# Performance work log

Hardware: AMD Instinct MI355X
Metric: run time of the kernel (lower is better)

Reference implementation:

```python
import jax, jax.numpy as jnp
import numpy as np

B, T, C, H = 2, 2048, 2048, 16
D = C // H  # head size = 128
ROPE_BASE = 10000.0


def setup_inputs() -> dict:
    key = jax.random.key(0)
    k1, k2, k3 = jax.random.split(key, 3)
    scale = 1.0 / np.sqrt(C)
    x = jax.random.normal(k1, (B, T, C), dtype=jnp.float32)
    w_qkv = jax.random.normal(k2, (3 * C, C), dtype=jnp.float32) * scale
    w_o = jax.random.normal(k3, (C, C), dtype=jnp.float32) * scale
    # rope cache: complex exp(i * pos * theta_j), stored as cos/sin, shape [T, D//2]
    inv_freq = 1.0 / (ROPE_BASE ** (np.arange(0, D, 2, dtype=np.float32) / D))  # [D//2]
    angles = np.arange(T, dtype=np.float32)[:, None] * inv_freq[None, :]        # [T, D//2]
    rope_cos = jnp.asarray(np.cos(angles))
    rope_sin = jnp.asarray(np.sin(angles))
    return {"x": x, "w_qkv": w_qkv, "w_o": w_o, "rope_cos": rope_cos, "rope_sin": rope_sin}


def _apply_rope(x, cos, sin):
    # x: [B, T, H, D]; cos/sin: [T, D//2]
    xr = x.reshape(*x.shape[:-1], D // 2, 2)
    x0, x1 = xr[..., 0], xr[..., 1]
    c = cos[None, :, None, :]
    s = sin[None, :, None, :]
    # complex multiply (x0 + i x1) * (c + i s)
    out = jnp.stack([x0 * c - x1 * s, x0 * s + x1 * c], axis=-1)
    return out.reshape(x.shape)


def reference(x, w_qkv, w_o, rope_cos, rope_sin):
    Bs, Ts, Cs = x.shape
    qkv = jnp.einsum('btc,ec->bte', x, w_qkv)  # [B, T, 3C]
    q, k, v = jnp.split(qkv, 3, axis=-1)
    q = q.reshape(Bs, Ts, H, D)
    k = k.reshape(Bs, Ts, H, D)
    v = v.reshape(Bs, Ts, H, D)
    q = _apply_rope(q, rope_cos[:Ts], rope_sin[:Ts])
    k = _apply_rope(k, rope_cos[:Ts], rope_sin[:Ts])
    scores = jnp.einsum('bthd,bshd->bhts', q, k) / jnp.sqrt(jnp.float32(D))
    causal = jnp.tril(jnp.ones((Ts, Ts), dtype=bool))
    scores = jnp.where(causal[None, None], scores, jnp.finfo(scores.dtype).min)
    attn = jax.nn.softmax(scores, axis=-1)
    y = jnp.einsum('bhts,bshd->bthd', attn, v).reshape(Bs, Ts, Cs)
    return jnp.einsum('btc,oc->bto', y, w_o)
```

## Files before the change

kernel.cpp:

```cpp
#include <hip/hip_runtime.h>
#include <cstdint>
#include <cstddef>

#define DEVI __device__ __forceinline__

typedef __attribute__((ext_vector_type(8))) short short8;
typedef __attribute__((ext_vector_type(4))) float f32x4;
typedef __attribute__((ext_vector_type(16))) float f32x16;
typedef __attribute__((ext_vector_type(4))) unsigned int u32x4;

static constexpr int Bdim = 2, T = 2048, C = 2048, H = 16, D = 128;
static constexpr int CQ = 3 * C;

DEVI unsigned short f2bf(float f) {
  unsigned int u = __float_as_uint(f);
  u = (u + 0x7fffu + ((u >> 16) & 1u)) >> 16;
  return (unsigned short)u;
}
DEVI float bf2f(unsigned int u) { return __uint_as_float(u << 16); }

DEVI unsigned int cvtpk(float lo, float hi) {
  unsigned int r;
  asm("v_cvt_pk_bf16_f32 %0, %1, %2" : "=v"(r) : "v"(lo), "v"(hi));
  return r;
}

DEVI void gload_lds16(const void* g, void* l) {
  __builtin_amdgcn_global_load_lds((const __attribute__((address_space(1))) void*)g,
                                   (__attribute__((address_space(3))) void*)l, 16, 0, 0);
}

__global__ __launch_bounds__(256) void convert_all(const float* __restrict__ x,
                                                   const float* __restrict__ wqkv,
                                                   const float* __restrict__ wo,
                                                   unsigned short* __restrict__ xb,
                                                   unsigned short* __restrict__ wqkvb,
                                                   unsigned short* __restrict__ wob) {
  int bid = blockIdx.x;
  const float* src;
  unsigned short* dst;
  if (bid < 8192) {
    src = x; dst = xb;
  } else if (bid < 8192 + 12288) {
    bid -= 8192; src = wqkv; dst = wqkvb;
  } else {
    bid -= 8192 + 12288; src = wo; dst = wob;
  }
  const int i = (bid * 256 + threadIdx.x) * 4;
  float4 v = *(const float4*)&src[i];
  uint2 o;
  o.x = (unsigned)f2bf(v.x) | ((unsigned)f2bf(v.y) << 16);
  o.y = (unsigned)f2bf(v.z) | ((unsigned)f2bf(v.w) << 16);
  *(uint2*)&dst[i] = o;
}

template <int OUT_BF16>
__global__ __launch_bounds__(256) void gemm_bt(const unsigned short* __restrict__ A,
                                               const unsigned short* __restrict__ Bm,
                                               void* __restrict__ outp,
                                               int M, int N, int Kd) {
  __shared__ __align__(16) unsigned short lds_a[128 * 64];
  __shared__ __align__(16) unsigned short lds_b[128 * 64];
  const int tid = threadIdx.x;
  const int wid = tid >> 6, lane = tid & 63;
  const int lg = lane >> 4, lc = lane & 15;
  const int m0 = blockIdx.y * 128, n0 = blockIdx.x * 128;
  const int wr = (wid >> 1) * 64, wc = (wid & 1) * 64;
  const int srow = wid * 8 + (lane >> 3);
  const int schunk = lane & 7;

  f32x4 acc[4][4] = {};

  for (int k0 = 0; k0 < Kd; k0 += 64) {
    __syncthreads();
#pragma unroll
    for (int j = 0; j < 4; ++j) {
      const int row = j * 32 + srow;
      const int cc = schunk ^ (row & 7);
      gload_lds16(&A[(size_t)(m0 + row) * Kd + k0 + cc * 8], &lds_a[j * 2048 + wid * 512]);
      gload_lds16(&Bm[(size_t)(n0 + row) * Kd + k0 + cc * 8], &lds_b[j * 2048 + wid * 512]);
    }
    __syncthreads();
    __builtin_amdgcn_s_setprio(1);
#pragma unroll
    for (int kk = 0; kk < 2; ++kk) {
      short8 af[4], bf[4];
#pragma unroll
      for (int m = 0; m < 4; ++m) {
        const int row = wr + m * 16 + lc;
        af[m] = *(const short8*)&lds_a[row * 64 + (((kk * 4 + lg) ^ (row & 7)) * 8)];
      }
#pragma unroll
      for (int n = 0; n < 4; ++n) {
        const int row = wc + n * 16 + lc;
        bf[n] = *(const short8*)&lds_b[row * 64 + (((kk * 4 + lg) ^ (row & 7)) * 8)];
      }
#pragma unroll
      for (int m = 0; m < 4; ++m)
#pragma unroll
        for (int n = 0; n < 4; ++n)
          acc[m][n] = __builtin_amdgcn_mfma_f32_16x16x32_bf16(af[m], bf[n], acc[m][n], 0, 0, 0);
    }
    __builtin_amdgcn_s_setprio(0);
  }

#pragma unroll
  for (int m = 0; m < 4; ++m)
#pragma unroll
    for (int n = 0; n < 4; ++n)
#pragma unroll
      for (int r = 0; r < 4; ++r) {
        const int row = m0 + wr + m * 16 + lg * 4 + r;
        const int col = n0 + wc + n * 16 + lc;
        const float v = acc[m][n][r];
        if (OUT_BF16)
          ((unsigned short*)outp)[(size_t)row * N + col] = f2bf(v);
        else
          ((float*)outp)[(size_t)row * N + col] = v;
      }
}

__global__ __launch_bounds__(256) void rope_vt_kernel(const unsigned short* __restrict__ qkv,
                                                      const float* __restrict__ cosb,
                                                      const float* __restrict__ sinb,
                                                      unsigned short* __restrict__ Qr,
                                                      unsigned short* __restrict__ Kr,
                                                      unsigned short* __restrict__ Vt) {
  if (blockIdx.x < 16384) {
    const int idx = blockIdx.x * 256 + threadIdx.x;
    const int i = idx & 63;
    const int h = (idx >> 6) & (H - 1);
    const int tg = idx >> 10;
    const int t = tg & (T - 1);
    const int b = tg >> 11;
    const float c = cosb[t * 64 + i], s = sinb[t * 64 + i];
    const unsigned short* row = qkv + (size_t)tg * CQ;
    const unsigned int q = *(const unsigned int*)&row[h * D + 2 * i];
    const unsigned int k = *(const unsigned int*)&row[C + h * D + 2 * i];
    const float q0 = bf2f(q & 0xffffu), q1 = bf2f(q >> 16);
    const float k0 = bf2f(k & 0xffffu), k1 = bf2f(k >> 16);
    const float SC = 0.08838834764831845f * 1.4426950408889634f;
    const float q0r = (q0 * c - q1 * s) * SC, q1r = (q0 * s + q1 * c) * SC;
    const float k0r = k0 * c - k1 * s, k1r = k0 * s + k1 * c;
    const size_t off = ((size_t)(b * H + h) * T + t) * D + 2 * i;
    *(unsigned int*)&Qr[off] = (unsigned)f2bf(q0r) | ((unsigned)f2bf(q1r) << 16);
    *(unsigned int*)&Kr[off] = (unsigned)f2bf(k0r) | ((unsigned)f2bf(k1r) << 16);
  } else {
    __shared__ unsigned short tile[64][65];
    const int bid2 = blockIdx.x - 16384;
    const int t0 = (bid2 & 31) * 64;
    const int d0 = ((bid2 >> 5) & 1) * 64;
    const int bh = bid2 >> 6, b = bh >> 4, h = bh & (H - 1);
    const int tx = threadIdx.x & 63, ty = threadIdx.x >> 6;
#pragma unroll
    for (int rr = 0; rr < 64; rr += 4)
      tile[rr + ty][tx] = qkv[(size_t)(b * T + t0 + rr + ty) * CQ + 2 * C + h * D + d0 + tx];
    __syncthreads();
#pragma unroll
    for (int rr = 0; rr < 64; rr += 4)
      Vt[((size_t)bh * D + d0 + rr + ty) * T + t0 + tx] = tile[tx][rr + ty];
  }
}

__global__ __launch_bounds__(256, 2) void flash_attn(const unsigned short* __restrict__ Q,
                                                     const unsigned short* __restrict__ K,
                                                     const unsigned short* __restrict__ Vt,
                                                     unsigned short* __restrict__ OA,
                                                     unsigned short* __restrict__ OB,
                                                     float2* __restrict__ ml) {
  __shared__ __align__(16) unsigned short ldsK[64 * 128];
  __shared__ __align__(16) unsigned short ldsV[64 * 128];

  const int bid = blockIdx.x;
  const int lid = (bid & 7) * 128 + (bid >> 3);
  const int bh = lid >> 5;
  const int qt = 15 - ((lid >> 1) & 15);
  const int hf = lid & 1;
  const int wid = threadIdx.x >> 6;
  const int lane = threadIdx.x & 63;
  const int l31 = lane & 31, l15 = lane & 15;
  const int hi = lane >> 5;
  const int b = bh >> 4, h = bh & (H - 1);
  const int q0w = qt * 128 + wid * 32;
  const int qrow = q0w + l31;

  const unsigned short* Qh = Q + (size_t)bh * T * D;
  const unsigned short* Kh = K + (size_t)bh * T * D;
  const unsigned short* Vh = Vt + (size_t)bh * D * T;

  const int sr = lane >> 4;
  const int tstart = hf ? (qt + 1) : 0;
  const int tend = hf ? (2 * qt + 2) : (qt + 1);

  short8 qf[8];
#pragma unroll
  for (int ds = 0; ds < 8; ++ds)
    qf[ds] = *(const short8*)&Qh[(size_t)qrow * D + ds * 16 + hi * 8];

  f32x16 oacc[4] = {};
  float m_run = -1e30f, l_run = 0.f;

  u32x4 rK[4], rV[4];

#pragma unroll
  for (int j = 0; j < 4; ++j) {
    const int r0 = (wid * 4 + j) * 4;
    const int row = r0 + sr;
    const int cc = l15 ^ (row & 15);
    rK[j] = *(const u32x4*)&Kh[(size_t)(tstart * 64 + row) * D + cc * 8];
    const int d = row + ((cc >> 3) << 6);
    rV[j] = *(const u32x4*)&Vh[(size_t)d * T + tstart * 64 + (cc & 7) * 8];
  }

  for (int t = tstart; t < tend; ++t) {
    const int kv0 = t * 64;

    __builtin_amdgcn_s_barrier();

#pragma unroll
    for (int j = 0; j < 4; ++j) {
      const int r0 = (wid * 4 + j) * 4;
      *(u32x4*)((char*)ldsK + r0 * 256 + lane * 16) = rK[j];
      *(u32x4*)((char*)ldsV + r0 * 256 + lane * 16) = rV[j];
    }
    asm volatile("s_waitcnt lgkmcnt(0)" ::: "memory");
    __builtin_amdgcn_s_barrier();
    __builtin_amdgcn_sched_barrier(0);

    if (t + 1 < tend) {
      const int kvn = kv0 + 64;
#pragma unroll
      for (int j = 0; j < 4; ++j) {
        const int r0 = (wid * 4 + j) * 4;
        const int row = r0 + sr;
        const int cc = l15 ^ (row & 15);
        rK[j] = *(const u32x4*)&Kh[(size_t)(kvn + row) * D + cc * 8];
        const int d = row + ((cc >> 3) << 6);
        rV[j] = *(const u32x4*)&Vh[(size_t)d * T + kvn + (cc & 7) * 8];
      }
    }
    __builtin_amdgcn_sched_barrier(0);

    if (kv0 <= q0w + 31) {
      f32x16 s0 = {}, s1 = {};
      __builtin_amdgcn_s_setprio(1);
#pragma unroll
      for (int ds = 0; ds < 8; ++ds) {
        const int cs = ((ds * 2 + hi) ^ l15) * 8;
        const short8 k0 = *(const short8*)&ldsK[l31 * 128 + cs];
        const short8 k1 = *(const short8*)&ldsK[(32 + l31) * 128 + cs];
        s0 = __builtin_amdgcn_mfma_f32_32x32x16_bf16(k0, qf[ds], s0, 0, 0, 0);
        s1 = __builtin_amdgcn_mfma_f32_32x32x16_bf16(k1, qf[ds], s1, 0, 0, 0);
      }
      __builtin_amdgcn_s_setprio(0);

      if (kv0 + 63 > q0w) {
#pragma unroll
        for (int r = 0; r < 16; ++r) {
          const int kvr = kv0 + (r & 3) + 8 * (r >> 2) + 4 * hi;
          s0[r] = (kvr <= qrow) ? s0[r] : -1e30f;
          s1[r] = (kvr + 32 <= qrow) ? s1[r] : -1e30f;
        }
      }

      float mt[8];
#pragma unroll
      for (int r = 0; r < 8; ++r)
        mt[r] = fmaxf(fmaxf(s0[r], s0[r + 8]), fmaxf(s1[r], s1[r + 8]));
#pragma unroll
      for (int r = 0; r < 4; ++r) mt[r] = fmaxf(mt[r], mt[r + 4]);
      float mx = fmaxf(fmaxf(mt[0], mt[1]), fmaxf(mt[2], mt[3]));
      mx = fmaxf(mx, __shfl_xor(mx, 32));
      const float mnew = fmaxf(m_run, mx);
      if (__any(mnew > m_run)) {
        const float f = exp2f(m_run - mnew);
        m_run = mnew;
        l_run *= f;
#pragma unroll
        for (int blk = 0; blk < 4; ++blk) oacc[blk] *= f;
      }
#pragma unroll
      for (int r = 0; r < 16; ++r) {
        s0[r] = exp2f(s0[r] - m_run);
        s1[r] = exp2f(s1[r] - m_run);
      }
      {
        float a0 = 0.f, a1 = 0.f, a2 = 0.f, a3 = 0.f;
#pragma unroll
        for (int r = 0; r < 16; r += 4) {
          a0 += s0[r] + s1[r];
          a1 += s0[r + 1] + s1[r + 1];
          a2 += s0[r + 2] + s1[r + 2];
          a3 += s0[r + 3] + s1[r + 3];
        }
        l_run += (a0 + a1) + (a2 + a3);
      }

      __builtin_amdgcn_s_setprio(1);
#pragma unroll
      for (int ks = 0; ks < 4; ++ks) {
        const int rb = (ks & 1) * 8;
        const f32x16& S = (ks < 2) ? s0 : s1;
        const unsigned int w0 = cvtpk(S[rb + 0], S[rb + 1]);
        const unsigned int w1 = cvtpk(S[rb + 2], S[rb + 3]);
        const unsigned int w2 = cvtpk(S[rb + 4], S[rb + 5]);
        const unsigned int w3 = cvtpk(S[rb + 6], S[rb + 7]);
        const unsigned int x0 = (unsigned int)__shfl_xor((int)w0, 32);
        const unsigned int x1 = (unsigned int)__shfl_xor((int)w1, 32);
        const unsigned int x2 = (unsigned int)__shfl_xor((int)w2, 32);
        const unsigned int x3 = (unsigned int)__shfl_xor((int)w3, 32);
        u32x4 av;
        av[0] = hi ? x2 : w0;
        av[1] = hi ? x3 : w1;
        av[2] = hi ? w2 : x0;
        av[3] = hi ? w3 : x1;
        const short8 pf = __builtin_bit_cast(short8, av);
#pragma unroll
        for (int blk = 0; blk < 4; ++blk) {
          const int row2 = (blk & 1) * 32 + l31;
          const int cs = ((((blk >> 1) * 8) + ks * 2 + hi) ^ l15) * 8;
          const short8 vf = *(const short8*)&ldsV[row2 * 128 + cs];
          oacc[blk] = __builtin_amdgcn_mfma_f32_32x32x16_bf16(vf, pf, oacc[blk], 0, 0, 0);
        }
      }
      __builtin_amdgcn_s_setprio(0);
    }
  }

  const float l = l_run + __shfl_xor(l_run, 32);
  const float inv = (l > 0.f) ? (1.0f / l) : 0.f;
  unsigned short* yrow = (hf ? OB : OA) + ((size_t)(b * T + qrow)) * C + h * D;
#pragma unroll
  for (int blk = 0; blk < 4; ++blk)
#pragma unroll
    for (int g = 0; g < 4; ++g) {
      const int d0 = blk * 32 + 8 * g + 4 * hi;
      uint2 st;
      st.x = cvtpk(oacc[blk][4 * g + 0] * inv, oacc[blk][4 * g + 1] * inv);
      st.y = cvtpk(oacc[blk][4 * g + 2] * inv, oacc[blk][4 * g + 3] * inv);
      *(uint2*)&yrow[d0] = st;
    }
  if (hi == 0) {
    float2 v;
    v.x = m_run;
    v.y = l;
    ml[(size_t)hf * (Bdim * H * T) + (size_t)bh * T + qrow] = v;
  }
}

__global__ __launch_bounds__(256) void combine_halves(const unsigned short* __restrict__ OA,
                                                      const unsigned short* __restrict__ OB,
                                                      const float2* __restrict__ ml,
                                                      unsigned short* __restrict__ Y) {
  const int i = blockIdx.x * 256 + threadIdx.x;
  const int d0 = (i & 15) * 8;
  const int rowid = i >> 4;
  const int bh = rowid >> 11, t = rowid & (T - 1);
  const int b = bh >> 4, h = bh & (H - 1);
  const float2 a = ml[rowid];
  const float2 bb = ml[(size_t)(Bdim * H * T) + rowid];
  const float m = fmaxf(a.x, bb.x);
  const float wA = a.y * exp2f(a.x - m);
  const float wB = bb.y * exp2f(bb.x - m);
  const float den = wA + wB;
  const float fA = wA / den, fB = wB / den;
  const size_t off = ((size_t)(b * T + t)) * C + h * D + d0;
  const u32x4 ra = *(const u32x4*)&OA[off];
  const u32x4 rb = *(const u32x4*)&OB[off];
  u32x4 w;
#pragma unroll
  for (int e = 0; e < 4; ++e) {
    const float o0 = bf2f(ra[e] & 0xffffu) * fA + bf2f(rb[e] & 0xffffu) * fB;
    const float o1 = bf2f(ra[e] >> 16) * fA + bf2f(rb[e] >> 16) * fB;
    w[e] = cvtpk(o0, o1);
  }
  *(u32x4*)&Y[off] = w;
}

extern "C" void kernel_launch(void* const* d_in, const int* in_sizes, int n_in,
                              void* d_out, int out_size, void* d_ws, size_t ws_size,
                              hipStream_t stream) {
  const float* x = (const float*)d_in[0];
  const float* wqkv = (const float*)d_in[1];
  const float* wo = (const float*)d_in[2];
  const float* rc = (const float*)d_in[3];
  const float* rs = (const float*)d_in[4];
  float* out = (float*)d_out;
  char* ws = (char*)d_ws;

  unsigned short* xb    = (unsigned short*)(ws + 0);
  unsigned short* wqkvb = (unsigned short*)(ws + 16777216);
  unsigned short* qkv   = (unsigned short*)(ws + 41943040);
  unsigned short* Qr    = (unsigned short*)(ws + 92274688);
  unsigned short* Kr    = (unsigned short*)(ws + 109051904);
  unsigned short* wob   = (unsigned short*)(ws + 125829120);
  unsigned short* Vt  = xb;
  unsigned short* OA  = (unsigned short*)(ws + 41943040);
  unsigned short* OB  = (unsigned short*)(ws + 58720256);
  float2*         ml  = (float2*)(ws + 75497472);
  unsigned short* Yf  = Qr;

  convert_all<<<8192 + 12288 + 4096, 256, 0, stream>>>(x, wqkv, wo, xb, wqkvb, wob);
  gemm_bt<1><<<dim3(CQ / 128, (Bdim * T) / 128), 256, 0, stream>>>(xb, wqkvb, (void*)qkv,
                                                                   Bdim * T, CQ, C);
  rope_vt_kernel<<<18432, 256, 0, stream>>>(qkv, rc, rs, Qr, Kr, Vt);
  flash_attn<<<1024, 256, 0, stream>>>(Qr, Kr, Vt, OA, OB, ml);
  combine_halves<<<4096, 256, 0, stream>>>(OA, OB, ml, Yf);
  gemm_bt<0><<<dim3(C / 128, (Bdim * T) / 128), 256, 0, stream>>>(Yf, wob, (void*)out,
                                                                  Bdim * T, C, C);
}
```

Measured before the change: 262.0 us.

## Double-buffer LDS tiles in bf16 GEMM to overlap global loads with MFMA

The GEMM kernel now keeps two LDS buffers for the A and B tiles. It prefetches the next K-slice directly into the alternate buffer while the MFMAs run on the current one, and it does a single wait plus barrier per iteration instead of two syncthreads. This is meant to hide global-to-LDS load latency behind the matrix math in the QKV and output projections. In exchange, LDS use per block doubles to 64KB, which can lower occupancy.

```diff
diff --git a/kernel.cpp b/kernel.cpp
--- a/kernel.cpp
+++ b/kernel.cpp
@@ -59,8 +59,8 @@
                                                const unsigned short* __restrict__ Bm,
                                                void* __restrict__ outp,
                                                int M, int N, int Kd) {
-  __shared__ __align__(16) unsigned short lds_a[128 * 64];
-  __shared__ __align__(16) unsigned short lds_b[128 * 64];
+  __shared__ __align__(16) unsigned short lds_a[2][128 * 64];
+  __shared__ __align__(16) unsigned short lds_b[2][128 * 64];
   const int tid = threadIdx.x;
   const int wid = tid >> 6, lane = tid & 63;
   const int lg = lane >> 4, lc = lane & 15;
@@ -71,16 +71,33 @@
 
   f32x4 acc[4][4] = {};
 
+#pragma unroll
+  for (int j = 0; j < 4; ++j) {
+    const int row = j * 32 + srow;
+    const int cc = schunk ^ (row & 7);
+    gload_lds16(&A[(size_t)(m0 + row) * Kd + cc * 8], &lds_a[0][j * 2048 + wid * 512]);
+    gload_lds16(&Bm[(size_t)(n0 + row) * Kd + cc * 8], &lds_b[0][j * 2048 + wid * 512]);
+  }
+
+  int cur = 0;
   for (int k0 = 0; k0 < Kd; k0 += 64) {
-    __syncthreads();
-#pragma unroll
-    for (int j = 0; j < 4; ++j) {
-      const int row = j * 32 + srow;
-      const int cc = schunk ^ (row & 7);
-      gload_lds16(&A[(size_t)(m0 + row) * Kd + k0 + cc * 8], &lds_a[j * 2048 + wid * 512]);
-      gload_lds16(&Bm[(size_t)(n0 + row) * Kd + k0 + cc * 8], &lds_b[j * 2048 + wid * 512]);
-    }
-    __syncthreads();
+    asm volatile("s_waitcnt vmcnt(0)" ::: "memory");
+    __builtin_amdgcn_s_barrier();
+    __builtin_amdgcn_sched_barrier(0);
+
+    if (k0 + 64 < Kd) {
+#pragma unroll
+      for (int j = 0; j < 4; ++j) {
+        const int row = j * 32 + srow;
+        const int cc = schunk ^ (row & 7);
+        gload_lds16(&A[(size_t)(m0 + row) * Kd + k0 + 64 + cc * 8],
+                    &lds_a[cur ^ 1][j * 2048 + wid * 512]);
+        gload_lds16(&Bm[(size_t)(n0 + row) * Kd + k0 + 64 + cc * 8],
+                    &lds_b[cur ^ 1][j * 2048 + wid * 512]);
+      }
+    }
+    __builtin_amdgcn_sched_barrier(0);
+
     __builtin_amdgcn_s_setprio(1);
 #pragma unroll
     for (int kk = 0; kk < 2; ++kk) {
@@ -88,12 +105,12 @@
 #pragma unroll
       for (int m = 0; m < 4; ++m) {
         const int row = wr + m * 16 + lc;
-        af[m] = *(const short8*)&lds_a[row * 64 + (((kk * 4 + lg) ^ (row & 7)) * 8)];
+        af[m] = *(const short8*)&lds_a[cur][row * 64 + (((kk * 4 + lg) ^ (row & 7)) * 8)];
       }
 #pragma unroll
       for (int n = 0; n < 4; ++n) {
         const int row = wc + n * 16 + lc;
-        bf[n] = *(const short8*)&lds_b[row * 64 + (((kk * 4 + lg) ^ (row & 7)) * 8)];
+        bf[n] = *(const short8*)&lds_b[cur][row * 64 + (((kk * 4 + lg) ^ (row & 7)) * 8)];
       }
 #pragma unroll
       for (int m = 0; m < 4; ++m)
@@ -102,6 +119,7 @@
           acc[m][n] = __builtin_amdgcn_mfma_f32_16x16x32_bf16(af[m], bf[n], acc[m][n], 0, 0, 0);
     }
     __builtin_amdgcn_s_setprio(0);
+    cur ^= 1;
   }
 
 #pragma unroll
```

After: 271.4 us. +3.6%, slower.

## Double-buffer GEMM LDS tiles with K=32 steps to overlap loads and MFMA

Applied to the files above, without the earlier changes.

Restructures the bf16 GEMM main loop to use two LDS buffers of 128x32 per operand. The next K-slice is prefetched via global-to-LDS loads while MFMAs run on the current slice, with a single wait and barrier per iteration. The swizzle changes to fit 32-wide rows. The K step halves, so there are twice as many barriers, and each prefetch is still fully drained (vmcnt(0)) at the top of the next iteration, which limits how much latency it can hide.

```diff
diff --git a/kernel.cpp b/kernel.cpp
--- a/kernel.cpp
+++ b/kernel.cpp
@@ -59,49 +59,64 @@
                                                const unsigned short* __restrict__ Bm,
                                                void* __restrict__ outp,
                                                int M, int N, int Kd) {
-  __shared__ __align__(16) unsigned short lds_a[128 * 64];
-  __shared__ __align__(16) unsigned short lds_b[128 * 64];
+  __shared__ __align__(16) unsigned short lds_a[2][128 * 32];
+  __shared__ __align__(16) unsigned short lds_b[2][128 * 32];
   const int tid = threadIdx.x;
   const int wid = tid >> 6, lane = tid & 63;
   const int lg = lane >> 4, lc = lane & 15;
   const int m0 = blockIdx.y * 128, n0 = blockIdx.x * 128;
   const int wr = (wid >> 1) * 64, wc = (wid & 1) * 64;
-  const int srow = wid * 8 + (lane >> 3);
-  const int schunk = lane & 7;
+  const int srow = lane >> 2;
+  const int sslot = lane & 3;
 
   f32x4 acc[4][4] = {};
 
-  for (int k0 = 0; k0 < Kd; k0 += 64) {
-    __syncthreads();
-#pragma unroll
-    for (int j = 0; j < 4; ++j) {
-      const int row = j * 32 + srow;
-      const int cc = schunk ^ (row & 7);
-      gload_lds16(&A[(size_t)(m0 + row) * Kd + k0 + cc * 8], &lds_a[j * 2048 + wid * 512]);
-      gload_lds16(&Bm[(size_t)(n0 + row) * Kd + k0 + cc * 8], &lds_b[j * 2048 + wid * 512]);
-    }
-    __syncthreads();
+#pragma unroll
+  for (int j = 0; j < 2; ++j) {
+    const int row = wid * 32 + j * 16 + srow;
+    const int cc = sslot ^ ((row >> 1) & 3);
+    gload_lds16(&A[(size_t)(m0 + row) * Kd + cc * 8], &lds_a[0][(wid * 32 + j * 16) * 32]);
+    gload_lds16(&Bm[(size_t)(n0 + row) * Kd + cc * 8], &lds_b[0][(wid * 32 + j * 16) * 32]);
+  }
+
+  int cur = 0;
+  for (int k0 = 0; k0 < Kd; k0 += 32) {
+    asm volatile("s_waitcnt vmcnt(0)" ::: "memory");
+    __builtin_amdgcn_s_barrier();
+    __builtin_amdgcn_sched_barrier(0);
+
+    if (k0 + 32 < Kd) {
+#pragma unroll
+      for (int j = 0; j < 2; ++j) {
+        const int row = wid * 32 + j * 16 + srow;
+        const int cc = sslot ^ ((row >> 1) & 3);
+        gload_lds16(&A[(size_t)(m0 + row) * Kd + k0 + 32 + cc * 8],
+                    &lds_a[cur ^ 1][(wid * 32 + j * 16) * 32]);
+        gload_lds16(&Bm[(size_t)(n0 + row) * Kd + k0 + 32 + cc * 8],
+                    &lds_b[cur ^ 1][(wid * 32 + j * 16) * 32]);
+      }
+    }
+    __builtin_amdgcn_sched_barrier(0);
+
     __builtin_amdgcn_s_setprio(1);
-#pragma unroll
-    for (int kk = 0; kk < 2; ++kk) {
-      short8 af[4], bf[4];
-#pragma unroll
-      for (int m = 0; m < 4; ++m) {
-        const int row = wr + m * 16 + lc;
-        af[m] = *(const short8*)&lds_a[row * 64 + (((kk * 4 + lg) ^ (row & 7)) * 8)];
-      }
-#pragma unroll
-      for (int n = 0; n < 4; ++n) {
-        const int row = wc + n * 16 + lc;
-        bf[n] = *(const short8*)&lds_b[row * 64 + (((kk * 4 + lg) ^ (row & 7)) * 8)];
-      }
-#pragma unroll
-      for (int m = 0; m < 4; ++m)
-#pragma unroll
-        for (int n = 0; n < 4; ++n)
-          acc[m][n] = __builtin_amdgcn_mfma_f32_16x16x32_bf16(af[m], bf[n], acc[m][n], 0, 0, 0);
-    }
+    short8 af[4], bf[4];
+#pragma unroll
+    for (int m = 0; m < 4; ++m) {
+      const int row = wr + m * 16 + lc;
+      af[m] = *(const short8*)&lds_a[cur][row * 32 + ((lg ^ ((row >> 1) & 3)) * 8)];
+    }
+#pragma unroll
+    for (int n = 0; n < 4; ++n) {
+      const int row = wc + n * 16 + lc;
+      bf[n] = *(const short8*)&lds_b[cur][row * 32 + ((lg ^ ((row >> 1) & 3)) * 8)];
+    }
+#pragma unroll
+    for (int m = 0; m < 4; ++m)
+#pragma unroll
+      for (int n = 0; n < 4; ++n)
+        acc[m][n] = __builtin_amdgcn_mfma_f32_16x16x32_bf16(af[m], bf[n], acc[m][n], 0, 0, 0);
     __builtin_amdgcn_s_setprio(0);
+    cur ^= 1;
   }
 
 #pragma unroll
```

Result: slower. 284.8 us (+8.7%).
